# Performance work log

Measured on AMD Instinct MI355X. Metric: run time of the kernel, lower is better.

## Reference

```python
import jax, jax.numpy as jnp
import numpy as np

N_NODES = 10000
N_EDGES = 640000
D = 128


def _sage_conv(x, src, dst, W_l, b, W_r):
    # PyG SAGEConv (mean aggr): out = lin_l(mean_{j in N(i)} x_j) + lin_r(x_i)
    msgs = x[src]                                        # [E, D_in] gather
    agg = jax.ops.segment_sum(msgs, dst, num_segments=N_NODES)  # [N, D_in]
    deg = jax.ops.segment_sum(jnp.ones((src.shape[0],), x.dtype), dst,
                              num_segments=N_NODES)
    agg = agg / jnp.maximum(deg, 1.0)[:, None]           # mean; isolated nodes -> 0
    return agg @ W_l + b + x @ W_r


def setup_inputs() -> dict:
    key = jax.random.key(0)
    ks = jax.random.split(key, 8)
    s = 1.0 / np.sqrt(D)
    return {
        "x": jax.random.normal(ks[0], (N_NODES, D), dtype=jnp.float32),
        "edge_index": jax.random.randint(ks[1], (2, N_EDGES), 0, N_NODES, dtype=jnp.int64),
        "W_l0": jax.random.normal(ks[2], (D, D), dtype=jnp.float32) * s,
        "b0": jnp.zeros((D,), dtype=jnp.float32),
        "W_r0": jax.random.normal(ks[3], (D, D), dtype=jnp.float32) * s,
        "W_l1": jax.random.normal(ks[4], (D, D), dtype=jnp.float32) * s,
        "b1": jnp.zeros((D,), dtype=jnp.float32),
        "W_r1": jax.random.normal(ks[5], (D, D), dtype=jnp.float32) * s,
    }


def reference(x, edge_index, W_l0, b0, W_r0, W_l1, b1, W_r1):
    # Dropout(p=0.3) is identity in eval mode (reference runs inference math).
    src, dst = edge_index[0], edge_index[1]
    h = jax.nn.elu(_sage_conv(x, src, dst, W_l0, b0, W_r0))
    h = jax.nn.elu(_sage_conv(h, src, dst, W_l1, b1, W_r1))
    return h
```

## Files before the change

### kernel.cpp

```cpp
#include <hip/hip_runtime.h>

#define N_NODES 10000
#define N_EDGES 640000
#define D 128
#define MAXDEG 128
#define NBUCK 157
#define BCAP 6144
#define EPT 5
#define ZROW 10000

typedef unsigned int uint;
typedef unsigned short u16;
typedef short bf16x8 __attribute__((ext_vector_type(8)));
typedef float f32x4 __attribute__((ext_vector_type(4)));

__device__ __forceinline__ u16 f2bf(float f) {
    uint u = __float_as_uint(f);
    return (u16)((u + 0x7fffu + ((u >> 16) & 1u)) >> 16);
}
__device__ __forceinline__ float bflo(uint v) { return __uint_as_float(v << 16); }
__device__ __forceinline__ float bfhi(uint v) { return __uint_as_float(v & 0xffff0000u); }

__device__ __forceinline__ int edge_at(const void* ei, int is32, int idx) {
    if (is32) return ((const int*)ei)[idx];
    return (int)((const long long*)ei)[idx];
}

__global__ __launch_bounds__(256)
void binp1_kernel(const void* __restrict__ ei, int* __restrict__ gcount,
                  uint* __restrict__ gbucket) {
    __shared__ int hist[NBUCK];
    __shared__ int base[NBUCK];
    __shared__ int s_is32;
    const int t = threadIdx.x;
    if (t < NBUCK) hist[t] = 0;
    if (t == 0) s_is32 = 0;
    __syncthreads();
    const int e0 = blockIdx.x * (256 * EPT);
    if (((const int*)ei)[2 * (e0 + t) + 1] != 0) s_is32 = 1;
    __syncthreads();
    const int is32 = s_is32;
    uint pk[EPT];
    int  rk[EPT];
#pragma unroll
    for (int i = 0; i < EPT; ++i) {
        int e  = e0 + i * 256 + t;
        int s  = edge_at(ei, is32, e);
        int dn = edge_at(ei, is32, N_EDGES + e);
        pk[i] = ((uint)dn << 16) | (uint)s;
        rk[i] = atomicAdd(&hist[dn >> 6], 1);
    }
    __syncthreads();
    if (t < NBUCK) base[t] = atomicAdd(&gcount[t], hist[t]);
    __syncthreads();
#pragma unroll
    for (int i = 0; i < EPT; ++i) {
        int bkt = (int)(pk[i] >> 22);
        int pos = base[bkt] + rk[i];
        if (pos < BCAP) gbucket[(size_t)bkt * BCAP + pos] = pk[i];
    }
}

__global__ __launch_bounds__(256)
void prep_kernel(const int* __restrict__ gcount, const uint* __restrict__ gbucket,
                 u16* __restrict__ adj, int* __restrict__ deg_g,
                 const float* __restrict__ x, uint* __restrict__ xb2,
                 uint* __restrict__ yb2,
                 const float* __restrict__ Wl0, const float* __restrict__ Wr0,
                 const float* __restrict__ Wl1, const float* __restrict__ Wr1,
                 u16* __restrict__ WT0, u16* __restrict__ WT1) {
    const int b = blockIdx.x;
    const int t = threadIdx.x;
    __shared__ __align__(16) u16 tile[64][MAXDEG];
    __shared__ int cur[64];
    if (b < NBUCK) {
        uint* tw = (uint*)&tile[0][0];
#pragma unroll
        for (int q = 0; q < 16; ++q) tw[t + q * 256] = ((uint)ZROW << 16) | ZROW;
        if (t < 64) cur[t] = 0;
        __syncthreads();
        const int total = min(gcount[b], BCAP);
        for (int e = t; e < total; e += 256) {
            uint pk = gbucket[(size_t)b * BCAP + e];
            int ln = (int)((pk >> 16) & 63u);
            int r = atomicAdd(&cur[ln], 1);
            if (r < MAXDEG) tile[ln][r] = (u16)(pk & 0xffffu);
        }
        __syncthreads();
        const int node0 = b * 64;
        if (t < 64 && node0 + t < N_NODES) deg_g[node0 + t] = cur[t];
        const uint4* ts = (const uint4*)&tile[0][0];
#pragma unroll
        for (int q = 0; q < 4; ++q) {
            int i = t + q * 256;
            int node = node0 + (i >> 4);
            if (node < N_NODES) ((uint4*)(adj + (size_t)node * MAXDEG))[i & 15] = ts[i];
        }
    } else if (b < NBUCK + 625) {
        int idx = (b - NBUCK) * 256 + t;
        const float4* p = (const float4*)x + (size_t)idx * 2;
        float4 a = p[0], bb = p[1];
        uint4 r;
        r.x = (uint)f2bf(a.x) | ((uint)f2bf(a.y) << 16);
        r.y = (uint)f2bf(a.z) | ((uint)f2bf(a.w) << 16);
        r.z = (uint)f2bf(bb.x) | ((uint)f2bf(bb.y) << 16);
        r.w = (uint)f2bf(bb.z) | ((uint)f2bf(bb.w) << 16);
        ((uint4*)xb2)[idx] = r;
    } else if (b < NBUCK + 625 + 256) {
        int b2 = b - (NBUCK + 625);
        int layer = b2 >> 7, d = b2 & 127, k = t;
        const float* Wl = layer ? Wl1 : Wl0;
        const float* Wr = layer ? Wr1 : Wr0;
        u16* WT = layer ? WT1 : WT0;
        float v = (k < 128) ? Wl[k * D + d] : Wr[(k - 128) * D + d];
        WT[(size_t)d * 256 + k] = f2bf(v);
    } else {
        if (t < 16) {
            ((uint4*)(xb2 + (size_t)ZROW * 64))[t] = make_uint4(0, 0, 0, 0);
            ((uint4*)(yb2 + (size_t)ZROW * 64))[t] = make_uint4(0, 0, 0, 0);
        }
    }
}

__global__ __launch_bounds__(1024, 8)
void fused_kernel(const uint* __restrict__ src2, const u16* __restrict__ adj,
                  const int* __restrict__ deg_g, const u16* __restrict__ WT,
                  const float* __restrict__ bias,
                  float* __restrict__ outf ,
                  u16* __restrict__ outb ) {
    __shared__ __align__(16) u16 A_lds[16 * 256];
    const int t = threadIdx.x;
    const int w = t >> 6, l = t & 63;
    const int nb = blockIdx.x * 16;
    const int node = nb + w;

    {
        const int g = l >> 4, c = l & 15;
        const int half = g >> 1, sh = (g & 1) << 4;
        const int dg = deg_g[node];
        const int cnt = min(dg, MAXDEG);
        const uint4* __restrict__ rowq = (const uint4*)(adj + (size_t)node * MAXDEG);
        float acc[8];
#pragma unroll
        for (int i = 0; i < 8; ++i) acc[i] = 0.f;
        const int nch = (cnt + 15) >> 4;
#pragma unroll 2
        for (int ch = 0; ch < nch; ++ch) {
            uint4 wa = rowq[2 * ch];
            uint4 wb = rowq[2 * ch + 1];
            uint a0 = half ? wa.y : wa.x;
            uint a1 = half ? wa.w : wa.z;
            uint b0 = half ? wb.y : wb.x;
            uint b1 = half ? wb.w : wb.z;
            uint id0 = (a0 >> sh) & 0xffffu;
            uint id1 = (a1 >> sh) & 0xffffu;
            uint id2 = (b0 >> sh) & 0xffffu;
            uint id3 = (b1 >> sh) & 0xffffu;
            uint4 v0 = ((const uint4*)(src2 + (size_t)id0 * 64))[c];
            uint4 v1 = ((const uint4*)(src2 + (size_t)id1 * 64))[c];
            uint4 v2 = ((const uint4*)(src2 + (size_t)id2 * 64))[c];
            uint4 v3 = ((const uint4*)(src2 + (size_t)id3 * 64))[c];
            acc[0] += bflo(v0.x) + bflo(v1.x) + bflo(v2.x) + bflo(v3.x);
            acc[1] += bfhi(v0.x) + bfhi(v1.x) + bfhi(v2.x) + bfhi(v3.x);
            acc[2] += bflo(v0.y) + bflo(v1.y) + bflo(v2.y) + bflo(v3.y);
            acc[3] += bfhi(v0.y) + bfhi(v1.y) + bfhi(v2.y) + bfhi(v3.y);
            acc[4] += bflo(v0.z) + bflo(v1.z) + bflo(v2.z) + bflo(v3.z);
            acc[5] += bfhi(v0.z) + bfhi(v1.z) + bfhi(v2.z) + bfhi(v3.z);
            acc[6] += bflo(v0.w) + bflo(v1.w) + bflo(v2.w) + bflo(v3.w);
            acc[7] += bfhi(v0.w) + bfhi(v1.w) + bfhi(v2.w) + bfhi(v3.w);
        }
#pragma unroll
        for (int i = 0; i < 8; ++i) {
            float r = acc[i];
            r += __shfl_xor(r, 16, 64);
            r += __shfl_xor(r, 32, 64);
            acc[i] = r;
        }
        char* arow = (char*)A_lds + w * 512;
        const int swz = (w & 7) << 4;
        if (g == 0) {
            float inv = 1.0f / fmaxf((float)dg, 1.0f);
            uint4 o;
            o.x = (uint)f2bf(acc[0] * inv) | ((uint)f2bf(acc[1] * inv) << 16);
            o.y = (uint)f2bf(acc[2] * inv) | ((uint)f2bf(acc[3] * inv) << 16);
            o.z = (uint)f2bf(acc[4] * inv) | ((uint)f2bf(acc[5] * inv) << 16);
            o.w = (uint)f2bf(acc[6] * inv) | ((uint)f2bf(acc[7] * inv) << 16);
            *(uint4*)(arow + ((c * 16) ^ swz)) = o;
        } else if (g == 1) {
            uint4 vx = ((const uint4*)(src2 + (size_t)node * 64))[c];
            *(uint4*)(arow + ((256 + c * 16) ^ swz)) = vx;
        }
    }
    __syncthreads();

    if (w < 8) {
        const int lr = l & 15, q = l >> 4;
        f32x4 acc0 = {0.f, 0.f, 0.f, 0.f};
        const u16* wt = WT + (size_t)(w * 16 + lr) * 256;
        const char* abase = (const char*)A_lds + lr * 512;
        const int aswz = (lr & 7) << 4;
#pragma unroll
        for (int kk = 0; kk < 8; ++kk) {
            bf16x8 af = *(const bf16x8*)(abase + ((kk * 64 + q * 16) ^ aswz));
            bf16x8 bf = *(const bf16x8*)(wt + kk * 32 + q * 8);
            acc0 = __builtin_amdgcn_mfma_f32_16x16x32_bf16(af, bf, acc0, 0, 0, 0);
        }
        const int col = w * 16 + lr;
        const float bv = bias[col];
#pragma unroll
        for (int j = 0; j < 4; ++j) {
            const int nd = nb + q * 4 + j;
            float v = acc0[j] + bv;
            v = v > 0.f ? v : expm1f(v);
            if (outf) outf[(size_t)nd * D + col] = v;
            if (outb) outb[(size_t)nd * D + col] = f2bf(v);
        }
    }
}

extern "C" void kernel_launch(void* const* d_in, const int* in_sizes, int n_in,
                              void* d_out, int out_size, void* d_ws, size_t ws_size,
                              hipStream_t stream) {
    const float* x   = (const float*)d_in[0];
    const void*  ei  = d_in[1];
    const float* Wl0 = (const float*)d_in[2];
    const float* b0  = (const float*)d_in[3];
    const float* Wr0 = (const float*)d_in[4];
    const float* Wl1 = (const float*)d_in[5];
    const float* b1  = (const float*)d_in[6];
    const float* Wr1 = (const float*)d_in[7];
    float* out = (float*)d_out;

    char* ws = (char*)d_ws;
    int*  gcount  = (int*)(ws + 1024);
    int*  deg     = (int*)(ws + 4096);
    u16*  adj     = (u16*)(ws + 65536);
    uint* gbucket = (uint*)(ws + 3145728);
    uint* xb2     = (uint*)(ws + 7340032);
    uint* yb2     = (uint*)(ws + 10485760);
    u16*  WT0     = (u16*)(ws + 13631488);
    u16*  WT1     = (u16*)(ws + 13697024);

    (void)hipMemsetAsync(ws, 0, 4096, stream);

    binp1_kernel<<<500, 256, 0, stream>>>(ei, gcount, gbucket);
    prep_kernel<<<NBUCK + 625 + 256 + 1, 256, 0, stream>>>(
        gcount, gbucket, adj, deg, x, xb2, yb2, Wl0, Wr0, Wl1, Wr1, WT0, WT1);

    fused_kernel<<<625, 1024, 0, stream>>>(xb2, adj, deg, WT0, b0,
                                           (float*)0, (u16*)yb2);
    fused_kernel<<<625, 1024, 0, stream>>>(yb2, adj, deg, WT1, b1,
                                           out, (u16*)0);
}
```

Baseline: 77.12 us.

## Vectorize edge loads, stage bucketed edges in LDS, prefetch adjacency chunks

The binning kernel now reads four edges per thread with 16-byte vector loads and scatters them into an LDS staging buffer sorted by bucket. It then writes them to global buckets in a mostly contiguous pattern, replacing scattered per-edge global stores. The fused aggregation kernel software-prefetches the next adjacency chunk and issues the self-row load early to hide latency. This adds a serial single-thread scan over 157 buckets and more LDS use in the binning kernel.

```diff
diff --git a/kernel.cpp b/kernel.cpp
--- a/kernel.cpp
+++ b/kernel.cpp
@@ -6,7 +6,7 @@
 #define MAXDEG 128
 #define NBUCK 157
 #define BCAP 6144
-#define EPT 5
+#define EPB2 1024
 #define ZROW 10000
 
 typedef unsigned int uint;
@@ -21,43 +21,60 @@
 __device__ __forceinline__ float bflo(uint v) { return __uint_as_float(v << 16); }
 __device__ __forceinline__ float bfhi(uint v) { return __uint_as_float(v & 0xffff0000u); }
 
-__device__ __forceinline__ int edge_at(const void* ei, int is32, int idx) {
-    if (is32) return ((const int*)ei)[idx];
-    return (int)((const long long*)ei)[idx];
-}
-
 __global__ __launch_bounds__(256)
 void binp1_kernel(const void* __restrict__ ei, int* __restrict__ gcount,
                   uint* __restrict__ gbucket) {
     __shared__ int hist[NBUCK];
-    __shared__ int base[NBUCK];
+    __shared__ int scan_[NBUCK];
+    __shared__ int gbase[NBUCK];
+    __shared__ uint stage[EPB2];
     __shared__ int s_is32;
     const int t = threadIdx.x;
     if (t < NBUCK) hist[t] = 0;
     if (t == 0) s_is32 = 0;
     __syncthreads();
-    const int e0 = blockIdx.x * (256 * EPT);
+    const int e0 = blockIdx.x * EPB2;
     if (((const int*)ei)[2 * (e0 + t) + 1] != 0) s_is32 = 1;
     __syncthreads();
     const int is32 = s_is32;
-    uint pk[EPT];
-    int  rk[EPT];
-#pragma unroll
-    for (int i = 0; i < EPT; ++i) {
-        int e  = e0 + i * 256 + t;
-        int s  = edge_at(ei, is32, e);
-        int dn = edge_at(ei, is32, N_EDGES + e);
-        pk[i] = ((uint)dn << 16) | (uint)s;
-        rk[i] = atomicAdd(&hist[dn >> 6], 1);
-    }
-    __syncthreads();
-    if (t < NBUCK) base[t] = atomicAdd(&gcount[t], hist[t]);
-    __syncthreads();
-#pragma unroll
-    for (int i = 0; i < EPT; ++i) {
-        int bkt = (int)(pk[i] >> 22);
-        int pos = base[bkt] + rk[i];
-        if (pos < BCAP) gbucket[(size_t)bkt * BCAP + pos] = pk[i];
+
+    uint srcs[4], dsts[4];
+    if (is32) {
+        uint4 s4 = ((const uint4*)ei)[(e0 >> 2) + t];
+        uint4 d4 = ((const uint4*)ei)[((N_EDGES + e0) >> 2) + t];
+        srcs[0] = s4.x; srcs[1] = s4.y; srcs[2] = s4.z; srcs[3] = s4.w;
+        dsts[0] = d4.x; dsts[1] = d4.y; dsts[2] = d4.z; dsts[3] = d4.w;
+    } else {
+        const uint4* p = (const uint4*)ei;
+        uint4 a  = p[(e0 >> 1) + 2 * t];
+        uint4 b2 = p[(e0 >> 1) + 2 * t + 1];
+        uint4 c4 = p[((N_EDGES + e0) >> 1) + 2 * t];
+        uint4 d4 = p[((N_EDGES + e0) >> 1) + 2 * t + 1];
+        srcs[0] = a.x;  srcs[1] = a.z;  srcs[2] = b2.x; srcs[3] = b2.z;
+        dsts[0] = c4.x; dsts[1] = c4.z; dsts[2] = d4.x; dsts[3] = d4.z;
+    }
+    uint pk[4]; int rk[4];
+#pragma unroll
+    for (int i = 0; i < 4; ++i) {
+        pk[i] = (dsts[i] << 16) | srcs[i];
+        rk[i] = atomicAdd(&hist[dsts[i] >> 6], 1);
+    }
+    __syncthreads();
+    if (t == 0) {
+        int c = 0;
+        for (int u = 0; u < NBUCK; ++u) { scan_[u] = c; c += hist[u]; }
+    }
+    __syncthreads();
+    if (t < NBUCK) gbase[t] = atomicAdd(&gcount[t], hist[t]);
+#pragma unroll
+    for (int i = 0; i < 4; ++i)
+        stage[scan_[(int)(dsts[i] >> 6)] + rk[i]] = pk[i];
+    __syncthreads();
+    for (int i = t; i < EPB2; i += 256) {
+        uint v = stage[i];
+        int bkt = (int)(v >> 22);
+        int pos = gbase[bkt] + (i - scan_[bkt]);
+        if (pos < BCAP) gbucket[(size_t)bkt * BCAP + pos] = v;
     }
 }
 
@@ -140,18 +157,24 @@
         const int dg = deg_g[node];
         const int cnt = min(dg, MAXDEG);
         const uint4* __restrict__ rowq = (const uint4*)(adj + (size_t)node * MAXDEG);
+        uint4 vx;
+        if (g == 1) vx = ((const uint4*)(src2 + (size_t)node * 64))[c];
         float acc[8];
 #pragma unroll
         for (int i = 0; i < 8; ++i) acc[i] = 0.f;
         const int nch = (cnt + 15) >> 4;
+        uint4 wa = rowq[0], wb = rowq[1];
 #pragma unroll 2
         for (int ch = 0; ch < nch; ++ch) {
-            uint4 wa = rowq[2 * ch];
-            uint4 wb = rowq[2 * ch + 1];
-            uint a0 = half ? wa.y : wa.x;
-            uint a1 = half ? wa.w : wa.z;
-            uint b0 = half ? wb.y : wb.x;
-            uint b1 = half ? wb.w : wb.z;
+            uint4 cwa = wa, cwb = wb;
+            if (ch + 1 < nch) {
+                wa = rowq[2 * ch + 2];
+                wb = rowq[2 * ch + 3];
+            }
+            uint a0 = half ? cwa.y : cwa.x;
+            uint a1 = half ? cwa.w : cwa.z;
+            uint b0 = half ? cwb.y : cwb.x;
+            uint b1 = half ? cwb.w : cwb.z;
             uint id0 = (a0 >> sh) & 0xffffu;
             uint id1 = (a1 >> sh) & 0xffffu;
             uint id2 = (b0 >> sh) & 0xffffu;
@@ -187,7 +210,6 @@
             o.w = (uint)f2bf(acc[6] * inv) | ((uint)f2bf(acc[7] * inv) << 16);
             *(uint4*)(arow + ((c * 16) ^ swz)) = o;
         } else if (g == 1) {
-            uint4 vx = ((const uint4*)(src2 + (size_t)node * 64))[c];
             *(uint4*)(arow + ((256 + c * 16) ^ swz)) = vx;
         }
     }
@@ -243,7 +265,7 @@
 
     (void)hipMemsetAsync(ws, 0, 4096, stream);
 
-    binp1_kernel<<<500, 256, 0, stream>>>(ei, gcount, gbucket);
+    binp1_kernel<<<625, 256, 0, stream>>>(ei, gcount, gbucket);
     prep_kernel<<<NBUCK + 625 + 256 + 1, 256, 0, stream>>>(
         gcount, gbucket, adj, deg, x, xb2, yb2, Wl0, Wr0, Wl1, Wr1, WT0, WT1);
 
```

Result: slower. 96.35 us (+24.9%).
